# Kernel tuning notes

Hardware: AMD Instinct MI355X
Metric: run time of the kernel (lower is better)

Reference implementation:

```python
import jax, jax.numpy as jnp
import numpy as np
from math import pi

N = 20000        # nodes
E = 640000       # edges (avg degree 32)
H = 128          # hidden_channels = num_filters
NB = 3           # num_bond_features
NGS = 50 - NB    # gaussians in smearing (num_gaussians - num_bond_features)
CUT = 10.0       # cutoff
L = 3            # num_interactions
B = 16           # graphs in batch
LOG2 = 0.6931471805599453


def ssp(x):
    # ShiftedSoftplus
    return jax.nn.softplus(x) - LOG2


def setup_inputs() -> dict:
    key = jax.random.key(0)
    ks = jax.random.split(key, 20)
    s = 0.05
    inp = {
        "z": jax.random.randint(ks[0], (N,), 0, 100),
        "pos": jax.random.uniform(ks[1], (N, 3), jnp.float32),
        "batch": jnp.sort(jax.random.randint(ks[2], (N,), 0, B)),
        "edge_index": jax.random.randint(ks[3], (2, E), 0, N),
        "edge_attr": jax.random.uniform(ks[4], (E, NB), jnp.float32),
        # parameters (stacked over L interaction blocks where per-layer)
        "emb": jax.random.normal(ks[5], (100, H), jnp.float32) * s,
        "mlp_w1": jax.random.normal(ks[6], (L, NB + NGS, H), jnp.float32) * s,
        "mlp_b1": jnp.zeros((L, H), jnp.float32),
        "mlp_w2": jax.random.normal(ks[7], (L, H, H), jnp.float32) * s,
        "mlp_b2": jnp.zeros((L, H), jnp.float32),
        "cf1_w": jax.random.normal(ks[8], (L, H, H), jnp.float32) * s,   # lin1, no bias
        "cf2_w": jax.random.normal(ks[9], (L, H, H), jnp.float32) * s,
        "cf2_b": jnp.zeros((L, H), jnp.float32),
        "lin_w": jax.random.normal(ks[10], (L, H, H), jnp.float32) * s,
        "lin_b": jnp.zeros((L, H), jnp.float32),
        "out1_w": jax.random.normal(ks[11], (H, H // 2), jnp.float32) * s,
        "out1_b": jnp.zeros((H // 2,), jnp.float32),
        "out2_w": jax.random.normal(ks[12], (H // 2, 1), jnp.float32) * s,
        "out2_b": jnp.zeros((1,), jnp.float32),
    }
    return inp


def reference(z, pos, batch, edge_index, edge_attr, emb,
              mlp_w1, mlp_b1, mlp_w2, mlp_b2,
              cf1_w, cf2_w, cf2_b, lin_w, lin_b,
              out1_w, out1_b, out2_w, out2_b):
    row, col = edge_index[0], edge_index[1]  # source j, target i
    h = emb[z]                               # [N,H] embedding_e(z)
    # edge_weight = ||pos[row] - pos[col]||
    ew = jnp.linalg.norm(pos[row] - pos[col], axis=-1)  # [E]
    # GaussianSmearing(0, cutoff, NGS)
    offset = jnp.linspace(0.0, CUT, NGS, dtype=jnp.float32)
    coeff = -0.5 / (offset[1] - offset[0]) ** 2
    gs = jnp.exp(coeff * (ew[:, None] - offset[None, :]) ** 2)  # [E,NGS]
    ea = jnp.concatenate([edge_attr, gs], axis=1)  # [E,50]
    # cosine cutoff weight
    C = 0.5 * (jnp.cos(ew * pi / CUT) + 1.0)       # [E]
    for l in range(L):
        # filter MLP on edge features
        W = ssp(ea @ mlp_w1[l] + mlp_b1[l]) @ mlp_w2[l] + mlp_b2[l]  # [E,H]
        W = W * C[:, None]
        xh = h @ cf1_w[l]                    # lin1 (no bias) [N,H]
        msg = xh[row] * W                    # gather-mul [E,H]
        agg = jax.ops.segment_sum(msg, col, num_segments=N)  # scatter-add [N,H]
        xc = agg @ cf2_w[l] + cf2_b[l]       # lin2
        xc = ssp(xc)
        xc = xc @ lin_w[l] + lin_b[l]        # block output lin
        h = h + xc                           # residual
    h = ssp(h @ out1_w + out1_b)             # [N,H/2]
    per_node = h @ out2_w + out2_b           # [N,1]
    out = jax.ops.segment_sum(per_node, batch, num_segments=B)  # readout 'add' -> [B,1]
    return out
```

## Files before the change

### kernel.cpp

```cpp
#include <hip/hip_runtime.h>
#include <hip/hip_bf16.h>

typedef __attribute__((ext_vector_type(8))) short bfrag;
typedef __attribute__((ext_vector_type(4))) float f32x4;

__device__ __forceinline__ float ssp_f(float x) {
    return fmaxf(x, 0.f) + __logf(1.f + __expf(-fabsf(x))) - 0.6931471805599453f;
}

__device__ __forceinline__ unsigned short f2b(float x) {
    __hip_bfloat16 h = __float2bfloat16(x);
    return *(unsigned short*)&h;
}

__global__ void sniff_kernel(const unsigned int* __restrict__ raw, int* __restrict__ flag)
{
    __shared__ int cnt[256];
    const int t = threadIdx.x;
    unsigned int w = raw[t];
    unsigned int e = (w >> 7) & 0xFFu;
    cnt[t] = (e >= 100u && e <= 135u) ? 1 : 0;
    __syncthreads();
    for (int s = 128; s > 0; s >>= 1) {
        if (t < s) cnt[t] += cnt[t + s];
        __syncthreads();
    }
    if (t == 0) *flag = (cnt[0] >= 160) ? 1 : 0;
}

__global__ void sniff_int_kernel(const unsigned int* __restrict__ z, int* __restrict__ iflag)
{
    __shared__ int cnt[128];
    const int t = threadIdx.x;
    cnt[t] = (z[2 * t + 1] == 0u) ? 1 : 0;
    __syncthreads();
    for (int s = 64; s > 0; s >>= 1) {
        if (t < s) cnt[t] += cnt[t + s];
        __syncthreads();
    }
    if (t == 0) *iflag = (cnt[0] >= 126) ? 1 : 0;
}

__global__ __launch_bounds__(256) void convert_kernel(
    const void* __restrict__ src, float* __restrict__ dst, int n,
    const int* __restrict__ flag)
{
    int i = blockIdx.x * 256 + threadIdx.x;
    if (i >= n) return;
    if (*flag) dst[i] = __bfloat162float(((const __hip_bfloat16*)src)[i]);
    else       dst[i] = ((const float*)src)[i];
}

__global__ __launch_bounds__(256) void convert_int_kernel(
    const void* __restrict__ src, int* __restrict__ dst, int n,
    const int* __restrict__ iflag)
{
    int i = blockIdx.x * 256 + threadIdx.x;
    if (i >= n) return;
    if (*iflag) dst[i] = (int)(((const long long*)src)[i]);
    else        dst[i] = ((const int*)src)[i];
}

__global__ __launch_bounds__(256) void embed_kernel(
    const int* __restrict__ z, const float* __restrict__ embf,
    float* __restrict__ h, int NH)
{
    int idx = blockIdx.x * 256 + threadIdx.x;
    if (idx >= NH) return;
    h[idx] = embf[z[idx >> 7] * 128 + (idx & 127)];
}

__global__ __launch_bounds__(256) void zero_int_kernel(int* p, int n)
{
    int i = blockIdx.x * 256 + threadIdx.x;
    if (i < n) p[i] = 0;
}

__global__ __launch_bounds__(256) void hist_kernel(const int* __restrict__ col,
                                                   int* __restrict__ count, int E)
{
    int e = blockIdx.x * 256 + threadIdx.x;
    if (e < E) atomicAdd(&count[col[e]], 1);
}

__global__ __launch_bounds__(256) void scan_kernel(const int* __restrict__ count,
                                                   int* __restrict__ rowptr,
                                                   int* __restrict__ next, int N)
{
    __shared__ int part[256];
    const int t = threadIdx.x;
    const int chunk = (N + 255) / 256;
    const int lo = t * chunk, hi = min(lo + chunk, N);
    int s = 0;
    for (int i = lo; i < hi; ++i) s += count[i];
    part[t] = s;
    __syncthreads();
    if (t == 0) {
        int run = 0;
        for (int i = 0; i < 256; ++i) { int v = part[i]; part[i] = run; run += v; }
        rowptr[N] = run;
    }
    __syncthreads();
    int run = part[t];
    for (int i = lo; i < hi; ++i) {
        rowptr[i] = run; next[i] = run;
        run += count[i];
    }
}

__global__ __launch_bounds__(256) void slot_kernel(const int* __restrict__ col,
                                                   int* __restrict__ next,
                                                   int* __restrict__ slot, int E)
{
    int e = blockIdx.x * 256 + threadIdx.x;
    if (e < E) slot[e] = atomicAdd(&next[col[e]], 1);
}

__global__ __launch_bounds__(256) void perm_kernel(const int* __restrict__ slot,
                                                   int* __restrict__ perm, int E)
{
    int e = blockIdx.x * 256 + threadIdx.x;
    if (e < E) perm[slot[e]] = e;
}

__global__ __launch_bounds__(256) void prep_edges_kernel(
    const float* __restrict__ posf, const int* __restrict__ row,
    const int* __restrict__ col, const float* __restrict__ eattrf,
    const int* __restrict__ perm,
    int* __restrict__ rowS, int* __restrict__ colS,
    float* __restrict__ CS, float* __restrict__ ewS,
    unsigned short* __restrict__ eaS, int E, int NB)
{
    int p = blockIdx.x * 256 + threadIdx.x;
    if (p >= E) return;
    const int e = perm[p];
    const int r = row[e], c = col[e];
    float dx = posf[r*3+0] - posf[c*3+0];
    float dy = posf[r*3+1] - posf[c*3+1];
    float dz = posf[r*3+2] - posf[c*3+2];
    float ew = sqrtf(dx*dx + dy*dy + dz*dz);
    rowS[p] = r; colS[p] = c; ewS[p] = ew;
    CS[p] = 0.5f * (cosf(ew * 0.3141592653589793f) + 1.0f);
    unsigned short* o = eaS + (long)p * 4;
    for (int q = 0; q < 4; ++q)
        o[q] = (q < NB) ? f2b(eattrf[(long)e * NB + q]) : (unsigned short)0;
}

__global__ __launch_bounds__(256) void wtrans_kernel(
    const float* __restrict__ src, unsigned short* __restrict__ dst,
    int K, int Kpad, int N)
{
    int idx = blockIdx.x * 256 + threadIdx.x;
    if (idx >= N * Kpad) return;
    int n = idx / Kpad, k = idx - n * Kpad;
    dst[idx] = (k < K) ? f2b(src[k * N + n]) : (unsigned short)0;
}

template<int MODE>
__global__ __launch_bounds__(256) void node_gemm_tiled(
    const float* __restrict__ in, const float* __restrict__ W,
    const float* __restrict__ bias, float* __restrict__ out, int N)
{
    __shared__ float in_s[32][128];
    const int t = threadIdx.x;
    const long n0 = (long)blockIdx.x * 32;
    for (int i = t; i < 32 * 128; i += 256) {
        long n = n0 + (i >> 7);
        in_s[i >> 7][i & 127] = (n < N) ? in[n * 128 + (i & 127)] : 0.f;
    }
    __syncthreads();
    const int j = t & 31, sub = t >> 5;
    const int c4 = j * 4, rb = sub * 4;
    float acc[4][4];
    float4 bv = make_float4(0.f, 0.f, 0.f, 0.f);
    if (MODE != 0) bv = *(const float4*)(bias + c4);
    #pragma unroll
    for (int i = 0; i < 4; ++i) { acc[i][0]=bv.x; acc[i][1]=bv.y; acc[i][2]=bv.z; acc[i][3]=bv.w; }
    #pragma unroll 4
    for (int k = 0; k < 128; ++k) {
        const float4 wv = *(const float4*)(W + k * 128 + c4);
        #pragma unroll
        for (int i = 0; i < 4; ++i) {
            const float a = in_s[rb + i][k];
            acc[i][0] += a * wv.x; acc[i][1] += a * wv.y;
            acc[i][2] += a * wv.z; acc[i][3] += a * wv.w;
        }
    }
    #pragma unroll
    for (int i = 0; i < 4; ++i) {
        long n = n0 + rb + i;
        if (n >= N) continue;
        float4 o;
        if (MODE == 1) {
            o.x = ssp_f(acc[i][0]); o.y = ssp_f(acc[i][1]);
            o.z = ssp_f(acc[i][2]); o.w = ssp_f(acc[i][3]);
        } else {
            o.x = acc[i][0]; o.y = acc[i][1]; o.z = acc[i][2]; o.w = acc[i][3];
        }
        if (MODE == 2) {
            float4 p = *(const float4*)(out + n * 128 + c4);
            o.x += p.x; o.y += p.y; o.z += p.z; o.w += p.w;
        }
        *(float4*)(out + n * 128 + c4) = o;
    }
}

__global__ __launch_bounds__(256) void edge_mfma(
    const int* __restrict__ rowS, const int* __restrict__ colS,
    const float* __restrict__ CS, const float* __restrict__ ewS,
    const unsigned short* __restrict__ eaS,
    const unsigned short* __restrict__ w1t, const float* __restrict__ b1,
    const unsigned short* __restrict__ w2t, const float* __restrict__ b2,
    const float* __restrict__ xh, float* __restrict__ agg,
    int E, int NB, int F50, float delta, float coeff)
{
    __shared__ __align__(16) short ea_b[32][64];
    __shared__ __align__(16) short t_b[32][128];
    __shared__ float runbuf[32][136];
    __shared__ int   row_s[32];
    __shared__ int   col_s[32];
    __shared__ float C_s[32];
    __shared__ float ew_s[32];
    __shared__ int   runcol_s[32];
    __shared__ int   runstart_s[33];
    __shared__ int   nruns_s;

    const int t = threadIdx.x;
    const long p0 = (long)blockIdx.x * 32;

    if (t < 32) {
        long p = p0 + t; if (p >= E) p = E - 1;
        row_s[t] = rowS[p];
        col_s[t] = colS[p];
        C_s[t]   = (p0 + t < E) ? CS[p] : 0.f;
        ew_s[t]  = ewS[p];
    }
    __syncthreads();
    if (t == 0) {
        int nr = 0;
        for (int i = 0; i < 32; ++i) {
            if (i == 0 || col_s[i] != col_s[i - 1]) {
                runcol_s[nr] = col_s[i];
                runstart_s[nr] = i;
                ++nr;
            }
        }
        runstart_s[nr] = 32;
        nruns_s = nr;
    }
    for (int i = t; i < 32 * 64; i += 256) {
        const int e = i >> 6, k = i & 63;
        long p = p0 + e; if (p >= E) p = E - 1;
        unsigned short v;
        if (k < NB)        v = eaS[p * 4 + k];
        else if (k < F50) {
            float d = ew_s[e] - (float)(k - NB) * delta;
            v = f2b(__expf(coeff * d * d));
        } else             v = 0;
        ea_b[e][k] = (short)v;
    }
    __syncthreads();

    const int lane = t & 63;
    const int w    = t >> 6;
    const int colL = lane & 15;
    const int quad = lane >> 4;
    const int m0   = (w & 1) * 16;

    {
        f32x4 acc[4];
        #pragma unroll
        for (int tt = 0; tt < 4; ++tt) acc[tt] = (f32x4){0.f, 0.f, 0.f, 0.f};
        #pragma unroll
        for (int ks = 0; ks < 2; ++ks) {
            const bfrag a = *(const bfrag*)&ea_b[m0 + colL][ks * 32 + quad * 8];
            #pragma unroll
            for (int tt = 0; tt < 4; ++tt) {
                const int n0 = ((w >> 1) * 4 + tt) * 16;
                const bfrag b = *(const bfrag*)&w1t[(long)(n0 + colL) * 64 + ks * 32 + quad * 8];
                acc[tt] = __builtin_amdgcn_mfma_f32_16x16x32_bf16(a, b, acc[tt], 0, 0, 0);
            }
        }
        #pragma unroll
        for (int tt = 0; tt < 4; ++tt) {
            const int n0 = ((w >> 1) * 4 + tt) * 16;
            const float bcol = b1[n0 + colL];
            #pragma unroll
            for (int reg = 0; reg < 4; ++reg) {
                float v = ssp_f(acc[tt][reg] + bcol);
                t_b[m0 + quad * 4 + reg][n0 + colL] = (short)f2b(v);
            }
        }
    }
    __syncthreads();

    {
        f32x4 acc[4];
        #pragma unroll
        for (int tt = 0; tt < 4; ++tt) acc[tt] = (f32x4){0.f, 0.f, 0.f, 0.f};
        #pragma unroll
        for (int ks = 0; ks < 4; ++ks) {
            const bfrag a = *(const bfrag*)&t_b[m0 + colL][ks * 32 + quad * 8];
            #pragma unroll
            for (int tt = 0; tt < 4; ++tt) {
                const int n0 = ((w >> 1) * 4 + tt) * 16;
                const bfrag b = *(const bfrag*)&w2t[(long)(n0 + colL) * 128 + ks * 32 + quad * 8];
                acc[tt] = __builtin_amdgcn_mfma_f32_16x16x32_bf16(a, b, acc[tt], 0, 0, 0);
            }
        }
        const int ebase = m0 + quad * 4;
        #pragma unroll
        for (int tt = 0; tt < 4; ++tt) {
            const int n0 = ((w >> 1) * 4 + tt) * 16;
            const int cg = n0 + colL;
            const float bcol = b2[cg];
            #pragma unroll
            for (int reg = 0; reg < 4; ++reg) {
                const int e = ebase + reg;
                const float v = acc[tt][reg] + bcol;
                runbuf[e][cg] = v * C_s[e] * xh[(long)row_s[e] * 128 + cg];
            }
        }
    }
    __syncthreads();

    const int nr = nruns_s;
    const int cc = t & 127;
    for (int r = t >> 7; r < nr; r += 2) {
        float a = 0.f;
        const int s1 = runstart_s[r + 1];
        for (int e = runstart_s[r]; e < s1; ++e)
            a += runbuf[e][cc];
        atomicAdd(&agg[(long)runcol_s[r] * 128 + cc], a);
    }
}

__global__ __launch_bounds__(256) void edge_atomic(
    const float* __restrict__ posf,
    const int* __restrict__ row, const int* __restrict__ col,
    const float* __restrict__ eattrf,
    const float* __restrict__ w1, const float* __restrict__ b1,
    const float* __restrict__ w2, const float* __restrict__ b2,
    const float* __restrict__ xh, float* __restrict__ agg,
    int E, int NB, int F50, float delta, float coeff)
{
    __shared__ float ea_s[32][52];
    __shared__ float t_s[32][128];
    __shared__ int   row_s[32];
    __shared__ int   col_s[32];
    __shared__ float C_s[32];
    __shared__ float ew_s[32];

    const int t = threadIdx.x;
    const long e0 = (long)blockIdx.x * 32;

    if (t < 32) {
        long e = e0 + t; if (e >= E) e = E - 1;
        const int r = row[e], c = col[e];
        row_s[t] = r; col_s[t] = c;
        float dx = posf[r*3+0] - posf[c*3+0];
        float dy = posf[r*3+1] - posf[c*3+1];
        float dz = posf[r*3+2] - posf[c*3+2];
        float ew = sqrtf(dx*dx + dy*dy + dz*dz);
        ew_s[t] = ew;
        C_s[t]  = (e0 + t < E) ? 0.5f * (cosf(ew * 0.3141592653589793f) + 1.0f) : 0.f;
        for (int q = 0; q < NB; ++q)
            ea_s[t][q] = eattrf[e * NB + q];
    }
    __syncthreads();
    {
        const int NGS = F50 - NB;
        for (int i = t; i < 32 * NGS; i += 256) {
            const int e = i / NGS, g = i - e * NGS;
            const float d = ew_s[e] - (float)g * delta;
            ea_s[e][NB + g] = __expf(coeff * d * d);
        }
    }
    __syncthreads();

    const int j = t & 31, sub = t >> 5;
    const int c4 = j * 4, eb = sub * 4;
    float acc[4][4];
    {
        const float4 bv = *(const float4*)(b1 + c4);
        #pragma unroll
        for (int i = 0; i < 4; ++i) { acc[i][0]=bv.x; acc[i][1]=bv.y; acc[i][2]=bv.z; acc[i][3]=bv.w; }
        for (int k = 0; k < F50; ++k) {
            const float4 wv = *(const float4*)(w1 + k * 128 + c4);
            #pragma unroll
            for (int i = 0; i < 4; ++i) {
                const float a = ea_s[eb + i][k];
                acc[i][0] += a * wv.x; acc[i][1] += a * wv.y;
                acc[i][2] += a * wv.z; acc[i][3] += a * wv.w;
            }
        }
        #pragma unroll
        for (int i = 0; i < 4; ++i) {
            float4 o;
            o.x = ssp_f(acc[i][0]); o.y = ssp_f(acc[i][1]);
            o.z = ssp_f(acc[i][2]); o.w = ssp_f(acc[i][3]);
            *(float4*)&t_s[eb + i][c4] = o;
        }
    }
    __syncthreads();
    {
        const float4 bv = *(const float4*)(b2 + c4);
        #pragma unroll
        for (int i = 0; i < 4; ++i) { acc[i][0]=bv.x; acc[i][1]=bv.y; acc[i][2]=bv.z; acc[i][3]=bv.w; }
        #pragma unroll 4
        for (int k = 0; k < 128; ++k) {
            const float4 wv = *(const float4*)(w2 + k * 128 + c4);
            #pragma unroll
            for (int i = 0; i < 4; ++i) {
                const float a = t_s[eb + i][k];
                acc[i][0] += a * wv.x; acc[i][1] += a * wv.y;
                acc[i][2] += a * wv.z; acc[i][3] += a * wv.w;
            }
        }
    }
    #pragma unroll
    for (int i = 0; i < 4; ++i) {
        const int e = eb + i;
        if (e0 + e >= E) continue;
        const float Ce = C_s[e];
        const float4 xv = *(const float4*)(xh + (long)row_s[e] * 128 + c4);
        float* ag = agg + (long)col_s[e] * 128 + c4;
        atomicAdd(ag + 0, acc[i][0] * Ce * xv.x);
        atomicAdd(ag + 1, acc[i][1] * Ce * xv.y);
        atomicAdd(ag + 2, acc[i][2] * Ce * xv.z);
        atomicAdd(ag + 3, acc[i][3] * Ce * xv.w);
    }
}

__global__ __launch_bounds__(128) void readout_simple(
    const float* __restrict__ h,
    const float* __restrict__ o1w, const float* __restrict__ o1b,
    const float* __restrict__ o2w, const float* __restrict__ o2b,
    const int* __restrict__ batch, float* __restrict__ accb)
{
    __shared__ float hr[128];
    __shared__ float vv[64];
    const int n = blockIdx.x;
    const int t = threadIdx.x;
    hr[t] = h[(long)n * 128 + t];
    __syncthreads();
    if (t < 64) {
        float a = o1b[t];
        #pragma unroll 8
        for (int k = 0; k < 128; ++k)
            a = fmaf(hr[k], o1w[k * 64 + t], a);
        vv[t] = ssp_f(a) * o2w[t];
    }
    __syncthreads();
    if (t < 32) vv[t] += vv[t + 32];
    __syncthreads();
    if (t < 16) vv[t] += vv[t + 16];
    __syncthreads();
    if (t < 8)  vv[t] += vv[t + 8];
    __syncthreads();
    if (t < 4)  vv[t] += vv[t + 4];
    __syncthreads();
    if (t < 2)  vv[t] += vv[t + 2];
    __syncthreads();
    if (t == 0) atomicAdd(&accb[batch[n]], vv[0] + vv[1] + o2b[0]);
}

__global__ void finalize_kernel(const float* __restrict__ accb,
                                float* __restrict__ out, int B)
{
    int t = blockIdx.x * 256 + threadIdx.x;
    if (t < B) out[t] = accb[t];
}

extern "C" void kernel_launch(void* const* d_in, const int* in_sizes, int n_in,
                              void* d_out, int out_size, void* d_ws, size_t ws_size,
                              hipStream_t stream)
{
    const int N   = in_sizes[0];
    const int E   = in_sizes[3] / 2;
    const int B   = out_size;
    const int H   = 128;
    const int L   = in_sizes[7] / H;
    const int NB  = in_sizes[4] / E;
    const int F50 = in_sizes[6] / (L * H);
    const int NGS = F50 - NB;
    const float delta = 10.0f / (float)(NGS - 1);
    const float coeff = -0.5f / (delta * delta);

    const int fidx[16] = {1, 4, 5, 6, 7, 8, 9, 10, 11, 12, 13, 14, 15, 16, 17, 18};
    long foff[17]; foff[0] = 0;
    for (int i = 0; i < 16; ++i) foff[i + 1] = foff[i] + in_sizes[fidx[i]];

    float* F = (float*)d_ws;
    long base = (foff[16] + 3) & ~3L;
    float* h    = F + base;
    float* xh   = h + (long)N * H;
    float* agg  = xh + (long)N * H;
    float* accb = agg + (long)N * H;
    int*   flag  = (int*)(accb + ((B + 3) & ~3));
    int*   iflag = flag + 1;
    int*   zi     = flag + 4;
    int*   batchi = zi + N;
    int*   eidxi  = batchi + N;
    int*   count  = eidxi + 2 * E;
    int*   rowptr = count + N;
    int*   next   = rowptr + N + 1;
    int*   slot   = next + N;
    int*   perm   = slot + E;
    int*   rowS   = perm + E;
    int*   colS   = rowS + E;
    float* CS     = (float*)(colS + E);
    float* ewS    = CS + E;
    unsigned short* eaS = (unsigned short*)(ewS + E);
    unsigned short* w1t = eaS + 4L * E;
    unsigned short* w2t = w1t + (long)L * 128 * 64;
    long used_bytes = (long)((char*)(w2t + (long)L * 128 * 128) - (char*)d_ws);
    const bool use_fast = (used_bytes <= (long)ws_size) && (F50 <= 64) && (NB <= 4);

    sniff_kernel<<<1, 256, 0, stream>>>((const unsigned int*)d_in[5], flag);
    sniff_int_kernel<<<1, 128, 0, stream>>>((const unsigned int*)d_in[0], iflag);

    for (int i = 0; i < 16; ++i) {
        int n = in_sizes[fidx[i]];
        convert_kernel<<<(n + 255) / 256, 256, 0, stream>>>(d_in[fidx[i]], F + foff[i], n, flag);
    }
    convert_int_kernel<<<(N + 255) / 256, 256, 0, stream>>>(d_in[0], zi, N, iflag);
    convert_int_kernel<<<(N + 255) / 256, 256, 0, stream>>>(d_in[2], batchi, N, iflag);
    convert_int_kernel<<<(2 * E + 255) / 256, 256, 0, stream>>>(d_in[3], eidxi, 2 * E, iflag);

    const float* posf   = F + foff[0];
    const float* eattrf = F + foff[1];
    const float* embf   = F + foff[2];
    const float* w1   = F + foff[3];  const float* b1   = F + foff[4];
    const float* w2   = F + foff[5];  const float* b2   = F + foff[6];
    const float* cf1  = F + foff[7];  const float* cf2  = F + foff[8];
    const float* cf2b = F + foff[9];  const float* lin  = F + foff[10];
    const float* linb = F + foff[11]; const float* o1   = F + foff[12];
    const float* o1b  = F + foff[13]; const float* o2   = F + foff[14];
    const float* o2b  = F + foff[15];

    if (use_fast) {
        zero_int_kernel<<<(N + 255) / 256, 256, 0, stream>>>(count, N);
        hist_kernel<<<(E + 255) / 256, 256, 0, stream>>>(eidxi + E, count, E);
        scan_kernel<<<1, 256, 0, stream>>>(count, rowptr, next, N);
        slot_kernel<<<(E + 255) / 256, 256, 0, stream>>>(eidxi + E, next, slot, E);
        perm_kernel<<<(E + 255) / 256, 256, 0, stream>>>(slot, perm, E);
        prep_edges_kernel<<<(E + 255) / 256, 256, 0, stream>>>(
            posf, eidxi, eidxi + E, eattrf, perm, rowS, colS, CS, ewS, eaS, E, NB);
        for (int l = 0; l < L; ++l) {
            wtrans_kernel<<<(128 * 64 + 255) / 256, 256, 0, stream>>>(
                w1 + (long)l * F50 * H, w1t + (long)l * 128 * 64, F50, 64, 128);
            wtrans_kernel<<<(128 * 128 + 255) / 256, 256, 0, stream>>>(
                w2 + (long)l * H * H, w2t + (long)l * 128 * 128, 128, 128, 128);
        }
    }

    embed_kernel<<<(N * H + 255) / 256, 256, 0, stream>>>(zi, embf, h, N * H);
    hipMemsetAsync(accb, 0, (size_t)B * sizeof(float), stream);

    const int ngemm = (N + 31) / 32;
    const int nedge = (E + 31) / 32;
    for (int l = 0; l < L; ++l) {
        hipMemsetAsync(agg, 0, (size_t)N * H * sizeof(float), stream);
        node_gemm_tiled<0><<<ngemm, 256, 0, stream>>>(h, cf1 + (long)l * H * H, nullptr, xh, N);
        if (use_fast) {
            edge_mfma<<<nedge, 256, 0, stream>>>(
                rowS, colS, CS, ewS, eaS,
                w1t + (long)l * 128 * 64, b1 + (long)l * H,
                w2t + (long)l * 128 * 128, b2 + (long)l * H,
                xh, agg, E, NB, F50, delta, coeff);
        } else {
            edge_atomic<<<nedge, 256, 0, stream>>>(
                posf, eidxi, eidxi + E, eattrf,
                w1 + (long)l * F50 * H, b1 + (long)l * H,
                w2 + (long)l * H * H,  b2 + (long)l * H,
                xh, agg, E, NB, F50, delta, coeff);
        }
        node_gemm_tiled<1><<<ngemm, 256, 0, stream>>>(agg, cf2 + (long)l * H * H, cf2b + (long)l * H, xh, N);
        node_gemm_tiled<2><<<ngemm, 256, 0, stream>>>(xh, lin + (long)l * H * H, linb + (long)l * H, h, N);
    }

    readout_simple<<<N, 128, 0, stream>>>(h, o1, o1b, o2, o2b, batchi, accb);
    finalize_kernel<<<(B + 255) / 256, 256, 0, stream>>>(accb, (float*)d_out, B);
}
```

Measured before the change: 1.531 ms.

## Build edge-feature MFMA fragments in registers and shrink edge kernel LDS

Each lane now generates its own A fragment for the first filter GEMM (bond attributes plus Gaussian smearing) directly in registers. This removes the ea_b LDS staging buffer and one block barrier. The message buffer runbuf is stored as bf16 instead of fp32, and t_b is padded to 136 columns, which cuts shared-memory use and avoids bank conflicts, so more blocks can be resident per CU. In exchange, the Gaussian exponentials are computed redundantly across waves, and the messages lose precision before the per-run summation and atomics.

After: 1.634 ms. 6.8% more time.

```diff
diff --git a/kernel.cpp b/kernel.cpp
--- a/kernel.cpp
+++ b/kernel.cpp
@@ -11,6 +11,11 @@
 __device__ __forceinline__ unsigned short f2b(float x) {
     __hip_bfloat16 h = __float2bfloat16(x);
     return *(unsigned short*)&h;
+}
+
+__device__ __forceinline__ float b2f(unsigned short u) {
+    unsigned int w = ((unsigned int)u) << 16;
+    return *(float*)&w;
 }
 
 __global__ void sniff_kernel(const unsigned int* __restrict__ raw, int* __restrict__ flag)
@@ -214,13 +219,11 @@
     const float* __restrict__ xh, float* __restrict__ agg,
     int E, int NB, int F50, float delta, float coeff)
 {
-    __shared__ __align__(16) short ea_b[32][64];
-    __shared__ __align__(16) short t_b[32][128];
-    __shared__ float runbuf[32][136];
+    __shared__ __align__(16) short t_b[32][136];
+    __shared__ unsigned short runbuf[32][136];
     __shared__ int   row_s[32];
     __shared__ int   col_s[32];
     __shared__ float C_s[32];
-    __shared__ float ew_s[32];
     __shared__ int   runcol_s[32];
     __shared__ int   runstart_s[33];
     __shared__ int   nruns_s;
@@ -233,31 +236,18 @@
         row_s[t] = rowS[p];
         col_s[t] = colS[p];
         C_s[t]   = (p0 + t < E) ? CS[p] : 0.f;
-        ew_s[t]  = ewS[p];
-    }
-    __syncthreads();
-    if (t == 0) {
-        int nr = 0;
-        for (int i = 0; i < 32; ++i) {
-            if (i == 0 || col_s[i] != col_s[i - 1]) {
-                runcol_s[nr] = col_s[i];
-                runstart_s[nr] = i;
-                ++nr;
-            }
-        }
-        runstart_s[nr] = 32;
-        nruns_s = nr;
-    }
-    for (int i = t; i < 32 * 64; i += 256) {
-        const int e = i >> 6, k = i & 63;
-        long p = p0 + e; if (p >= E) p = E - 1;
-        unsigned short v;
-        if (k < NB)        v = eaS[p * 4 + k];
-        else if (k < F50) {
-            float d = ew_s[e] - (float)(k - NB) * delta;
-            v = f2b(__expf(coeff * d * d));
-        } else             v = 0;
-        ea_b[e][k] = (short)v;
+        if (t == 0) {
+            int nr = 0;
+            for (int i = 0; i < 32; ++i) {
+                if (i == 0 || col_s[i] != col_s[i - 1]) {
+                    runcol_s[nr] = col_s[i];
+                    runstart_s[nr] = i;
+                    ++nr;
+                }
+            }
+            runstart_s[nr] = 32;
+            nruns_s = nr;
+        }
     }
     __syncthreads();
 
@@ -267,18 +257,33 @@
     const int quad = lane >> 4;
     const int m0   = (w & 1) * 16;
 
+    long pA = p0 + m0 + colL; if (pA >= E) pA = E - 1;
+    const float ew = ewS[pA];
+
     {
         f32x4 acc[4];
         #pragma unroll
         for (int tt = 0; tt < 4; ++tt) acc[tt] = (f32x4){0.f, 0.f, 0.f, 0.f};
         #pragma unroll
         for (int ks = 0; ks < 2; ++ks) {
-            const bfrag a = *(const bfrag*)&ea_b[m0 + colL][ks * 32 + quad * 8];
+            const int kb = ks * 32 + quad * 8;
+            union { bfrag v; unsigned short s[8]; } af;
+            #pragma unroll
+            for (int j = 0; j < 8; ++j) {
+                const int k = kb + j;
+                unsigned short u;
+                if (k < NB)        u = eaS[pA * 4 + k];
+                else if (k < F50) {
+                    float d = ew - (float)(k - NB) * delta;
+                    u = f2b(__expf(coeff * d * d));
+                } else             u = 0;
+                af.s[j] = u;
+            }
             #pragma unroll
             for (int tt = 0; tt < 4; ++tt) {
                 const int n0 = ((w >> 1) * 4 + tt) * 16;
-                const bfrag b = *(const bfrag*)&w1t[(long)(n0 + colL) * 64 + ks * 32 + quad * 8];
-                acc[tt] = __builtin_amdgcn_mfma_f32_16x16x32_bf16(a, b, acc[tt], 0, 0, 0);
+                const bfrag b = *(const bfrag*)&w1t[(long)(n0 + colL) * 64 + kb];
+                acc[tt] = __builtin_amdgcn_mfma_f32_16x16x32_bf16(af.v, b, acc[tt], 0, 0, 0);
             }
         }
         #pragma unroll
@@ -318,7 +323,7 @@
             for (int reg = 0; reg < 4; ++reg) {
                 const int e = ebase + reg;
                 const float v = acc[tt][reg] + bcol;
-                runbuf[e][cg] = v * C_s[e] * xh[(long)row_s[e] * 128 + cg];
+                runbuf[e][cg] = f2b(v * C_s[e] * xh[(long)row_s[e] * 128 + cg]);
             }
         }
     }
@@ -330,7 +335,7 @@
         float a = 0.f;
         const int s1 = runstart_s[r + 1];
         for (int e = runstart_s[r]; e < s1; ++e)
-            a += runbuf[e][cc];
+            a += b2f(runbuf[e][cc]);
         atomicAdd(&agg[(long)runcol_s[r] * 128 + cc], a);
     }
 }
```
